# Kernel optimization log

Hardware: AMD Instinct MI355X
Metric: run time of the kernel (lower is better)

## Reference

```python
import jax, jax.numpy as jnp
import numpy as np

B, S, N, D, H = 128, 512, 32, 512, 2  # batch, seq_len, num_size, node_dim, hop_size
NPAD = 4  # padded number slots per row


def _lin(key, fi, fo):
    return 0.02 * jax.random.normal(key, (H, fi, fo), jnp.float32), jnp.zeros((H, fo), jnp.float32)


def setup_inputs() -> dict:
    key = jax.random.key(0)
    ks = jax.random.split(key, 12)
    encoder_outputs = jax.random.normal(ks[0], (S, B, D), jnp.float32)
    num_encoder_outputs = jax.random.normal(ks[1], (B, N, D), jnp.float32)
    # distinct positions per row in [0, S), last NPAD slots padded with -1
    num_pos_pad = jnp.argsort(jax.random.uniform(ks[2], (B, S)), axis=-1)[:, :N].astype(jnp.int32)
    num_pos_pad = num_pos_pad.at[:, -NPAD:].set(-1)
    # order ranks 1..N (random permutation per row), 0 on padded slots
    num_order_pad = (jnp.argsort(jax.random.uniform(ks[3], (B, N)), axis=-1) + 1).astype(jnp.int32)
    num_order_pad = num_order_pad.at[:, -NPAD:].set(0)
    w_n1a, b_n1a = _lin(ks[4], D, D)
    w_n1b, b_n1b = _lin(ks[5], D, D)
    w_n2a, b_n2a = _lin(ks[6], D, D)
    w_n2b, b_n2b = _lin(ks[7], D, D)
    w_g, b_g = _lin(ks[8], 4 * D, D)
    w_o, b_o = _lin(ks[9], 2 * D, D)
    return dict(encoder_outputs=encoder_outputs, num_encoder_outputs=num_encoder_outputs,
                num_pos_pad=num_pos_pad, num_order_pad=num_order_pad,
                w_n1a=w_n1a, b_n1a=b_n1a, w_n1b=w_n1b, b_n1b=b_n1b,
                w_n2a=w_n2a, b_n2a=b_n2a, w_n2b=w_n2b, b_n2b=b_n2b,
                w_g=w_g, b_g=b_g, w_o=w_o, b_o=b_o)


def reference(encoder_outputs, num_encoder_outputs, num_pos_pad, num_order_pad,
              w_n1a, b_n1a, w_n1b, b_n1b, w_n2a, b_n2a, w_n2b, b_n2b,
              w_g, b_g, w_o, b_o):
    node_mask = (num_order_pad > 0)                              # [B,N]
    greater = num_order_pad[:, :, None] > num_order_pad[:, None, :]
    lower = ~greater                                             # <=
    eye = jnp.eye(N, dtype=jnp.float32)
    pair = (node_mask[:, None, :] & node_mask[:, :, None]).astype(jnp.float32) * (1.0 - eye)
    g_gt = pair * greater.astype(jnp.float32) + eye              # [B,N,N]
    g_lt = pair * lower.astype(jnp.float32) + eye
    # row-normalize (D^{-1} A); diagonal guarantees row sums >= 1
    g_gt = g_gt / g_gt.sum(-1, keepdims=True)
    g_lt = g_lt / g_lt.sum(-1, keepdims=True)

    node = num_encoder_outputs                                   # [B,N,D]
    for h in range(H):
        ni1 = jax.nn.relu(jnp.einsum('bnm,bmd,de->bne', g_gt, node, w_n1a[h]) + b_n1a[h])
        ni1 = jax.nn.relu(jnp.einsum('bnm,bmd,de->bne', g_gt, ni1, w_n1b[h]) + b_n1b[h])
        ni2 = jax.nn.relu(jnp.einsum('bnm,bmd,de->bne', g_lt, node, w_n2a[h]) + b_n2a[h])
        ni2 = jax.nn.relu(jnp.einsum('bnm,bmd,de->bne', g_lt, ni2, w_n2b[h]) + b_n2b[h])
        gate_in = jnp.concatenate([ni1, ni2, ni1 + ni2, ni1 - ni2], axis=-1)
        gate = jax.nn.sigmoid(gate_in @ w_g[h] + b_g[h])
        node_info = gate * ni1 + (1.0 - gate) * ni2
        node = jax.nn.relu(jnp.concatenate([node, node_info], axis=-1) @ w_o[h] + b_o[h])

    # scatter node embeddings into padded [B, S+1, D]; pads -> slot S (dropped)
    num_mask = num_pos_pad > -1
    clamped = jnp.where(num_mask, num_pos_pad, S)                # [B,N]
    gnn_info = jnp.zeros((B, S + 1, D), jnp.float32)
    gnn_info = gnn_info.at[jnp.arange(B)[:, None], clamped].set(node)
    gnn_info = gnn_info[:, :S, :].transpose(1, 0, 2)             # [S,B,D]
    gnn_info = encoder_outputs + gnn_info
    num_embedding = num_encoder_outputs + node
    problem_output = jnp.max(gnn_info, axis=0)                   # [B,D]
    return gnn_info, num_embedding, problem_output
```

## Files before the change

kernel.cpp:

```cpp
#include <hip/hip_runtime.h>
#include <math.h>

#define BB 128
#define SS 512
#define NN 32
#define DD 512
#define HH 2
#define MM (BB * NN)
#define DSQ (DD * DD)

typedef short bf16x8 __attribute__((ext_vector_type(8)));
typedef float f32x4 __attribute__((ext_vector_type(4)));

__device__ __forceinline__ unsigned short f2bf(float f) {
    unsigned int u = __float_as_uint(f);
    u += 0x7fffu + ((u >> 16) & 1u);
    return (unsigned short)(u >> 16);
}
__device__ __forceinline__ float bf2f(unsigned short h) {
    return __uint_as_float(((unsigned int)h) << 16);
}
__device__ __forceinline__ void g2l16(const void* gp, void* lp) {
    __builtin_amdgcn_global_load_lds(
        (const __attribute__((address_space(1))) void*)gp,
        (__attribute__((address_space(3))) void*)lp, 16, 0, 0);
}

__global__ __launch_bounds__(256) void adj_k(const int* __restrict__ order,
                                             const int* __restrict__ pos,
                                             float* __restrict__ g_gt,
                                             float* __restrict__ g_lt,
                                             int* __restrict__ slot) {
    int b = blockIdx.x;
    __shared__ int ord[NN];
    __shared__ float sgt[NN][NN + 1];
    __shared__ float slt[NN][NN + 1];
    __shared__ float rs_gt[NN], rs_lt[NN];
    int tid = threadIdx.x;
    slot[b * SS + tid] = -1;
    slot[b * SS + 256 + tid] = -1;
    if (tid < NN) ord[tid] = order[b * NN + tid];
    __syncthreads();
    for (int q = 0; q < 4; ++q) {
        int idx = tid + 256 * q;
        int n = idx >> 5, m = idx & 31;
        bool valid = (ord[n] > 0) && (ord[m] > 0) && (n != m);
        float eye = (n == m) ? 1.f : 0.f;
        bool gt = ord[n] > ord[m];
        sgt[n][m] = ((valid && gt) ? 1.f : 0.f) + eye;
        slt[n][m] = ((valid && !gt) ? 1.f : 0.f) + eye;
    }
    __syncthreads();
    if (tid < NN) {
        float s1 = 0.f, s2 = 0.f;
        for (int m = 0; m < NN; ++m) { s1 += sgt[tid][m]; s2 += slt[tid][m]; }
        rs_gt[tid] = s1; rs_lt[tid] = s2;
    }
    __syncthreads();
    for (int q = 0; q < 4; ++q) {
        int idx = tid + 256 * q;
        int n = idx >> 5, m = idx & 31;
        g_gt[b * 1024 + idx] = sgt[n][m] / rs_gt[n];
        g_lt[b * 1024 + idx] = slt[n][m] / rs_lt[n];
    }
    if (tid < NN) {
        int p = pos[b * NN + tid];
        if (p >= 0) slot[b * SS + p] = tid;
    }
}

struct WSfull { const float* s[12]; int slot[12]; const float* w_g; };

__global__ __launch_bounds__(256) void wprep_k(WSfull w, unsigned short* __restrict__ Wt) {
    int which = blockIdx.x;
    int tile = blockIdx.y;
    int tr = (tile >> 3) * 64, tc = (tile & 7) * 64;
    __shared__ float c1[64][65];
    __shared__ float c2[64][65];
    int lc = threadIdx.x & 63, g4 = threadIdx.x >> 6;
    if (which < 12) {
        const float* src = w.s[which];
        unsigned short* dst = Wt + (size_t)w.slot[which] * DSQ;
        for (int i = 0; i < 16; ++i) {
            int lr = g4 * 16 + i;
            c1[lr][lc] = src[(size_t)(tr + lr) * DD + tc + lc];
        }
        __syncthreads();
        for (int i = 0; i < 16; ++i) {
            int lr = g4 * 16 + i;
            dst[(size_t)(tc + lr) * DD + tr + lc] = f2bf(c1[lc][lr]);
        }
    } else {
        int h = which - 12;
        const float* base = w.w_g + (size_t)h * 4 * DSQ;
        for (int i = 0; i < 16; ++i) {
            int lr = g4 * 16 + i;
            int k = tr + lr, n = tc + lc;
            float a  = base[(size_t)k * DD + n];
            float b2 = base[(size_t)(DD + k) * DD + n];
            float c  = base[(size_t)(2 * DD + k) * DD + n];
            float d4 = base[(size_t)(3 * DD + k) * DD + n];
            c1[lr][lc] = a + c + d4;
            c2[lr][lc] = b2 + c - d4;
        }
        __syncthreads();
        unsigned short* d1 = Wt + (size_t)(h * 8 + 4) * DSQ;
        unsigned short* d2 = Wt + (size_t)(h * 8 + 5) * DSQ;
        for (int i = 0; i < 16; ++i) {
            int lr = g4 * 16 + i;
            d1[(size_t)(tc + lr) * DD + tr + lc] = f2bf(c1[lc][lr]);
            d2[(size_t)(tc + lr) * DD + tr + lc] = f2bf(c2[lc][lr]);
        }
    }
}

__global__ void conv_k(const float* __restrict__ x, unsigned short* __restrict__ o) {
    size_t i = ((size_t)blockIdx.x * 256 + threadIdx.x) * 4;
    float4 v = *(const float4*)(x + i);
    ushort4 r;
    r.x = f2bf(v.x); r.y = f2bf(v.y); r.z = f2bf(v.z); r.w = f2bf(v.w);
    *(ushort4*)(o + i) = r;
}

struct GA {
    const unsigned short* A1; const unsigned short* W1;
    const unsigned short* A2; const unsigned short* W2;
    const float* g; const float* bias;
    const unsigned short* gin1; const unsigned short* gin2;
    unsigned short* out;
};

template <bool MIX, bool DUAL, bool GATE>
__global__ __launch_bounds__(256) void mgemm_k(GA a0, GA a1) {
    GA g = (blockIdx.z == 0) ? a0 : a1;
    __shared__ __align__(16) unsigned short stag[8192];
    __shared__ float gsh[2048];
    const int tid = threadIdx.x;
    const int lane = tid & 63;
    const int wave = tid >> 6;
    const int wr = wave & 1, wc = wave >> 1;
    const int bm = blockIdx.x * 64, bn = blockIdx.y * 64;

    if (MIX) {
        const float4* gsrc = (const float4*)(g.g + (size_t)(bm >> 5) * 1024);
        ((float4*)gsh)[tid] = gsrc[tid];
        ((float4*)gsh)[tid + 256] = gsrc[tid + 256];
    }

    f32x4 acc[2][2];
#pragma unroll
    for (int i = 0; i < 2; ++i)
#pragma unroll
        for (int j = 0; j < 2; ++j) {
            acc[i][j].x = 0.f; acc[i][j].y = 0.f; acc[i][j].z = 0.f; acc[i][j].w = 0.f;
        }

    const int r0 = tid >> 3,          s0 = (tid & 7) ^ (r0 & 7);
    const int r1 = (tid + 256) >> 3,  s1 = (tid & 7) ^ (r1 & 7);
    unsigned short* As = stag;
    unsigned short* Bs = stag + 4096;
    unsigned short* dA0 = As + wave * 512;
    unsigned short* dA1 = As + 2048 + wave * 512;
    unsigned short* dB0 = Bs + wave * 512;
    unsigned short* dB1 = Bs + 2048 + wave * 512;

    int aoff[2][2], boff[2][2];
#pragma unroll
    for (int t = 0; t < 2; ++t)
#pragma unroll
        for (int i = 0; i < 2; ++i) {
            int s = t * 4 + (lane >> 4);
            int p = s ^ (lane & 7);
            int m = wr * 32 + i * 16 + (lane & 15);
            aoff[t][i] = m * 64 + p * 8;
            int n = wc * 32 + i * 16 + (lane & 15);
            boff[t][i] = n * 64 + p * 8;
        }

    const int nsrc = DUAL ? 2 : 1;
    for (int src = 0; src < nsrc; ++src) {
        const unsigned short* A = src ? g.A2 : g.A1;
        const unsigned short* W = src ? g.W2 : g.W1;
        const unsigned short* Ab0 = A + (size_t)(bm + r0) * DD + s0 * 8;
        const unsigned short* Ab1 = A + (size_t)(bm + r1) * DD + s1 * 8;
        const unsigned short* Wb0 = W + (size_t)(bn + r0) * DD + s0 * 8;
        const unsigned short* Wb1 = W + (size_t)(bn + r1) * DD + s1 * 8;
        for (int k0 = 0; k0 < DD; k0 += 64) {
            g2l16(Ab0 + k0, dA0);
            g2l16(Ab1 + k0, dA1);
            g2l16(Wb0 + k0, dB0);
            g2l16(Wb1 + k0, dB1);
            __syncthreads();
            bf16x8 af[2][2], bf_[2][2];
#pragma unroll
            for (int t = 0; t < 2; ++t)
#pragma unroll
                for (int i = 0; i < 2; ++i) {
                    af[t][i]  = *(const bf16x8*)(As + aoff[t][i]);
                    bf_[t][i] = *(const bf16x8*)(Bs + boff[t][i]);
                }
#pragma unroll
            for (int t = 0; t < 2; ++t)
#pragma unroll
                for (int i = 0; i < 2; ++i)
#pragma unroll
                    for (int j = 0; j < 2; ++j)
                        acc[i][j] = __builtin_amdgcn_mfma_f32_16x16x32_bf16(
                            af[t][i], bf_[t][j], acc[i][j], 0, 0, 0);
            __syncthreads();
        }
    }

    if (!MIX) {
#pragma unroll
        for (int i = 0; i < 2; ++i) {
            int row = bm + wr * 32 + i * 16 + (lane >> 4) * 4;
#pragma unroll
            for (int j = 0; j < 2; ++j) {
                int col = bn + wc * 32 + j * 16 + (lane & 15);
                float bv = g.bias[col];
#pragma unroll
                for (int rg = 0; rg < 4; ++rg) {
                    float v = acc[i][j][rg] + bv;
                    size_t idx = (size_t)(row + rg) * DD + col;
                    if (GATE) {
                        float gg = 1.f / (1.f + __expf(-v));
                        float x1 = bf2f(g.gin1[idx]);
                        float x2 = bf2f(g.gin2[idx]);
                        g.out[idx] = f2bf(gg * x1 + (1.f - gg) * x2);
                    } else {
                        g.out[idx] = f2bf(fmaxf(v, 0.f));
                    }
                }
            }
        }
    } else {
        float* S = (float*)stag;
#pragma unroll
        for (int i = 0; i < 2; ++i) {
            int row = wr * 32 + i * 16 + (lane >> 4) * 4;
#pragma unroll
            for (int j = 0; j < 2; ++j) {
                int col = wc * 32 + j * 16 + (lane & 15);
#pragma unroll
                for (int rg = 0; rg < 4; ++rg) S[(row + rg) * 64 + col] = acc[i][j][rg];
            }
        }
        __syncthreads();
#pragma unroll
        for (int t = 0; t < 4; ++t) {
            int task = t * 256 + tid;
            int n = task >> 4, dq = task & 15;
            int bt = n >> 5, nl = n & 31;
            float r0m = 0.f, r1m = 0.f, r2m = 0.f, r3m = 0.f;
            const float* gr = gsh + bt * 1024 + nl * 32;
            const float* Sb = S + bt * 32 * 64 + dq * 4;
#pragma unroll
            for (int m = 0; m < 32; ++m) {
                float gv = gr[m];
                f32x4 sv = *(const f32x4*)(Sb + m * 64);
                r0m += gv * sv.x; r1m += gv * sv.y; r2m += gv * sv.z; r3m += gv * sv.w;
            }
            float4 bv = *(const float4*)(g.bias + bn + dq * 4);
            ushort4 ov;
            ov.x = f2bf(fmaxf(r0m + bv.x, 0.f));
            ov.y = f2bf(fmaxf(r1m + bv.y, 0.f));
            ov.z = f2bf(fmaxf(r2m + bv.z, 0.f));
            ov.w = f2bf(fmaxf(r3m + bv.w, 0.f));
            *(ushort4*)(g.out + (size_t)(bm + n) * DD + bn + dq * 4) = ov;
        }
    }
}

__global__ __launch_bounds__(256) void gnn_k(const float* __restrict__ enc,
                                             const unsigned short* __restrict__ node,
                                             const int* __restrict__ slot,
                                             const float* __restrict__ num_enc,
                                             float* __restrict__ out_gnn,
                                             float* __restrict__ out_nemb,
                                             float* __restrict__ partial) {
    int b = blockIdx.x;
    int t = threadIdx.x;
    if (blockIdx.y >= 16) {
        int q = blockIdx.y - 16;
        size_t base = (size_t)b * NN * DD + (size_t)q * (NN * DD / 4);
        for (int it = 0; it < 4; ++it) {
            size_t i = base + (size_t)(it * 256 + t) * 4;
            float4 a = *(const float4*)(num_enc + i);
            ushort4 nb = *(const ushort4*)(node + i);
            float4 r;
            r.x = a.x + bf2f(nb.x);
            r.y = a.y + bf2f(nb.y);
            r.z = a.z + bf2f(nb.z);
            r.w = a.w + bf2f(nb.w);
            *(float4*)(out_nemb + i) = r;
        }
        return;
    }
    __shared__ int sl[32];
    __shared__ float4 red[128];
    int s0 = blockIdx.y * 32;
    if (t < 32) sl[t] = slot[b * SS + s0 + t];
    __syncthreads();
    const int dv = (t & 127) * 4;
    const int sh = t >> 7;
    float4 mx = {-INFINITY, -INFINITY, -INFINITY, -INFINITY};
#pragma unroll 4
    for (int i = 0; i < 16; ++i) {
        int sloc = sh * 16 + i;
        int s = s0 + sloc;
        int n = sl[sloc];
        size_t ebase = ((size_t)s * BB + b) * DD + dv;
        float4 v = *(const float4*)(enc + ebase);
        if (n >= 0) {
            ushort4 nb = *(const ushort4*)(node + ((size_t)b * NN + n) * DD + dv);
            v.x += bf2f(nb.x);
            v.y += bf2f(nb.y);
            v.z += bf2f(nb.z);
            v.w += bf2f(nb.w);
        }
        *(float4*)(out_gnn + ebase) = v;
        mx.x = fmaxf(mx.x, v.x);
        mx.y = fmaxf(mx.y, v.y);
        mx.z = fmaxf(mx.z, v.z);
        mx.w = fmaxf(mx.w, v.w);
    }
    if (sh == 1) red[t & 127] = mx;
    __syncthreads();
    if (sh == 0) {
        float4 o = red[t];
        mx.x = fmaxf(mx.x, o.x);
        mx.y = fmaxf(mx.y, o.y);
        mx.z = fmaxf(mx.z, o.z);
        mx.w = fmaxf(mx.w, o.w);
        *(float4*)(partial + ((size_t)b * 16 + blockIdx.y) * DD + dv) = mx;
    }
}

__global__ void pmax_k(const float* __restrict__ partial, float* __restrict__ out_prob) {
    int i = blockIdx.x * 256 + threadIdx.x;
    if (i >= BB * DD) return;
    int b = i >> 9, d = i & 511;
    float m = -INFINITY;
    for (int c = 0; c < 16; ++c) m = fmaxf(m, partial[((size_t)b * 16 + c) * DD + d]);
    out_prob[i] = m;
}

extern "C" void kernel_launch(void* const* d_in, const int* in_sizes, int n_in,
                              void* d_out, int out_size, void* d_ws, size_t ws_size,
                              hipStream_t stream) {
    const float* enc     = (const float*)d_in[0];
    const float* num_enc = (const float*)d_in[1];
    const int*   pos     = (const int*)d_in[2];
    const int*   order   = (const int*)d_in[3];
    const float* w_n1a = (const float*)d_in[4];  const float* b_n1a = (const float*)d_in[5];
    const float* w_n1b = (const float*)d_in[6];  const float* b_n1b = (const float*)d_in[7];
    const float* w_n2a = (const float*)d_in[8];  const float* b_n2a = (const float*)d_in[9];
    const float* w_n2b = (const float*)d_in[10]; const float* b_n2b = (const float*)d_in[11];
    const float* w_g   = (const float*)d_in[12]; const float* b_g   = (const float*)d_in[13];
    const float* w_o   = (const float*)d_in[14]; const float* b_o   = (const float*)d_in[15];

    char* wp = (char*)d_ws;
    float* g_gt = (float*)wp;        wp += (size_t)BB * NN * NN * 4;
    float* g_lt = (float*)wp;        wp += (size_t)BB * NN * NN * 4;
    float* partial = (float*)wp;     wp += (size_t)BB * 16 * DD * 4;
    int* slot = (int*)wp;            wp += (size_t)BB * SS * 4;
    unsigned short* Wt = (unsigned short*)wp;    wp += (size_t)16 * DSQ * 2;
    unsigned short* node0 = (unsigned short*)wp; wp += (size_t)MM * DD * 2;
    unsigned short* nodeA = (unsigned short*)wp; wp += (size_t)MM * DD * 2;
    unsigned short* nodeB = (unsigned short*)wp; wp += (size_t)MM * DD * 2;
    unsigned short* ni1 = (unsigned short*)wp;   wp += (size_t)MM * DD * 2;
    unsigned short* ni2 = (unsigned short*)wp;   wp += (size_t)MM * DD * 2;
    unsigned short* t1 = (unsigned short*)wp;    wp += (size_t)MM * DD * 2;
    unsigned short* t2 = (unsigned short*)wp;    wp += (size_t)MM * DD * 2;

    float* out_gnn  = (float*)d_out;
    float* out_nemb = out_gnn + (size_t)SS * BB * DD;
    float* out_prob = out_nemb + (size_t)BB * NN * DD;

    adj_k<<<BB, 256, 0, stream>>>(order, pos, g_gt, g_lt, slot);

    WSfull wsrc;
    const float* srcs[12] = {w_n1a, w_n1b, w_n2a, w_n2b, w_o, w_o + DSQ,
                             w_n1a + DSQ, w_n1b + DSQ, w_n2a + DSQ, w_n2b + DSQ,
                             w_o + 2 * DSQ, w_o + 3 * DSQ};
    int slots[12] = {0, 1, 2, 3, 6, 7, 8, 9, 10, 11, 14, 15};
    for (int i = 0; i < 12; ++i) { wsrc.s[i] = srcs[i]; wsrc.slot[i] = slots[i]; }
    wsrc.w_g = w_g;
    wprep_k<<<dim3(14, 64), 256, 0, stream>>>(wsrc, Wt);
    conv_k<<<(MM * DD) / 1024, 256, 0, stream>>>(num_enc, node0);

    dim3 dgrid(MM / 64, DD / 64, 2);
    dim3 sgrid(MM / 64, DD / 64, 1);

    const unsigned short* nodeIn = node0;
    for (int h = 0; h < HH; ++h) {
        unsigned short* nodeOut = (h == 0) ? nodeA : nodeB;
        const unsigned short* Wh = Wt + (size_t)h * 8 * DSQ;

        GA sa0 = {nodeIn, Wh + 0 * DSQ, nullptr, nullptr, g_gt, b_n1a + h * DD,
                  nullptr, nullptr, ni1};
        GA sa1 = {nodeIn, Wh + 2 * DSQ, nullptr, nullptr, g_lt, b_n2a + h * DD,
                  nullptr, nullptr, ni2};
        mgemm_k<true, false, false><<<dgrid, 256, 0, stream>>>(sa0, sa1);

        GA sb0 = {ni1, Wh + 1 * DSQ, nullptr, nullptr, g_gt, b_n1b + h * DD,
                  nullptr, nullptr, t1};
        GA sb1 = {ni2, Wh + 3 * DSQ, nullptr, nullptr, g_lt, b_n2b + h * DD,
                  nullptr, nullptr, t2};
        mgemm_k<true, false, false><<<dgrid, 256, 0, stream>>>(sb0, sb1);

        GA gg = {t1, Wh + 4 * DSQ, t2, Wh + 5 * DSQ, nullptr, b_g + h * DD, t1, t2, ni1};
        mgemm_k<false, true, true><<<sgrid, 256, 0, stream>>>(gg, gg);

        GA go = {nodeIn, Wh + 6 * DSQ, ni1, Wh + 7 * DSQ, nullptr, b_o + h * DD,
                 nullptr, nullptr, nodeOut};
        mgemm_k<false, true, false><<<sgrid, 256, 0, stream>>>(go, go);

        nodeIn = nodeOut;
    }
    const unsigned short* nodeF = nodeIn;

    gnn_k<<<dim3(BB, 20), 256, 0, stream>>>(enc, nodeF, slot, num_enc,
                                            out_gnn, out_nemb, partial);
    pmax_k<<<(BB * DD) / 256, 256, 0, stream>>>(partial, out_prob);
}
```

Before: 412.1 us.

## Split adjacency mixing into separate kernel and enlarge GEMM tiles to 128x128

Moves the per-batch adjacency mixing (G @ X) out of the GEMM epilogue into a standalone mix_k kernel that runs before each GEMM. The mixing order changes from (X W) then G to (G X) then W. This lets the GEMM tiles grow from 64x64 to 128x128 with a 4x4 MFMA accumulator per wave, which raises data reuse per loaded tile. In exchange it adds two extra kernel launches per hop plus an extra bf16 round trip for the mixed activations. The larger tiles also use more registers and LDS and leave only 256 or 128 blocks per GEMM.

```diff
diff --git a/kernel.cpp b/kernel.cpp
--- a/kernel.cpp
+++ b/kernel.cpp
@@ -122,58 +122,111 @@
     *(ushort4*)(o + i) = r;
 }
 
+__global__ __launch_bounds__(256) void mix_k(const float* __restrict__ g_gt,
+                                             const float* __restrict__ g_lt,
+                                             const unsigned short* __restrict__ X1,
+                                             const unsigned short* __restrict__ X2,
+                                             unsigned short* __restrict__ Z1,
+                                             unsigned short* __restrict__ Z2) {
+    const int b = blockIdx.x;
+    const int dc = blockIdx.y * 128;
+    const float* G = blockIdx.z ? g_lt : g_gt;
+    const unsigned short* X = blockIdx.z ? X2 : X1;
+    unsigned short* Z = blockIdx.z ? Z2 : Z1;
+    __shared__ float gs[NN * 33];
+    __shared__ float xs[NN][128];
+    const int t = threadIdx.x;
+    {
+        float4 v = ((const float4*)(G + (size_t)b * 1024))[t];
+        int n = t >> 3, m0 = (t & 7) * 4;
+        float* gp = gs + n * 33 + m0;
+        gp[0] = v.x; gp[1] = v.y; gp[2] = v.z; gp[3] = v.w;
+    }
+#pragma unroll
+    for (int q = 0; q < 2; ++q) {
+        int e = t + 256 * q;
+        int m = e >> 4, c = (e & 15) * 8;
+        const unsigned short* src = X + ((size_t)(b * NN + m)) * DD + dc + c;
+        ushort4 lo = *(const ushort4*)src;
+        ushort4 hi = *(const ushort4*)(src + 4);
+        float* xp = &xs[m][c];
+        xp[0] = bf2f(lo.x); xp[1] = bf2f(lo.y); xp[2] = bf2f(lo.z); xp[3] = bf2f(lo.w);
+        xp[4] = bf2f(hi.x); xp[5] = bf2f(hi.y); xp[6] = bf2f(hi.z); xp[7] = bf2f(hi.w);
+    }
+    __syncthreads();
+    const int n = t >> 3;
+    const int c0 = (t & 7) * 16;
+    f32x4 r0 = {0.f, 0.f, 0.f, 0.f}, r1 = r0, r2 = r0, r3 = r0;
+#pragma unroll
+    for (int m = 0; m < NN; ++m) {
+        float gv = gs[n * 33 + m];
+        const float* xr = &xs[m][c0];
+        r0 += gv * *(const f32x4*)(xr);
+        r1 += gv * *(const f32x4*)(xr + 4);
+        r2 += gv * *(const f32x4*)(xr + 8);
+        r3 += gv * *(const f32x4*)(xr + 12);
+    }
+    unsigned short* dst = Z + ((size_t)(b * NN + n)) * DD + dc + c0;
+    ushort4 o0, o1, o2, o3;
+    o0.x = f2bf(r0.x); o0.y = f2bf(r0.y); o0.z = f2bf(r0.z); o0.w = f2bf(r0.w);
+    o1.x = f2bf(r1.x); o1.y = f2bf(r1.y); o1.z = f2bf(r1.z); o1.w = f2bf(r1.w);
+    o2.x = f2bf(r2.x); o2.y = f2bf(r2.y); o2.z = f2bf(r2.z); o2.w = f2bf(r2.w);
+    o3.x = f2bf(r3.x); o3.y = f2bf(r3.y); o3.z = f2bf(r3.z); o3.w = f2bf(r3.w);
+    *(ushort4*)(dst)      = o0;
+    *(ushort4*)(dst + 4)  = o1;
+    *(ushort4*)(dst + 8)  = o2;
+    *(ushort4*)(dst + 12) = o3;
+}
+
 struct GA {
     const unsigned short* A1; const unsigned short* W1;
     const unsigned short* A2; const unsigned short* W2;
-    const float* g; const float* bias;
+    const float* bias;
     const unsigned short* gin1; const unsigned short* gin2;
     unsigned short* out;
 };
 
-template <bool MIX, bool DUAL, bool GATE>
+template <bool DUAL, bool GATE>
 __global__ __launch_bounds__(256) void mgemm_k(GA a0, GA a1) {
     GA g = (blockIdx.z == 0) ? a0 : a1;
-    __shared__ __align__(16) unsigned short stag[8192];
-    __shared__ float gsh[2048];
+    __shared__ __align__(16) unsigned short As[128 * 64];
+    __shared__ __align__(16) unsigned short Bs[128 * 64];
     const int tid = threadIdx.x;
     const int lane = tid & 63;
     const int wave = tid >> 6;
     const int wr = wave & 1, wc = wave >> 1;
-    const int bm = blockIdx.x * 64, bn = blockIdx.y * 64;
-
-    if (MIX) {
-        const float4* gsrc = (const float4*)(g.g + (size_t)(bm >> 5) * 1024);
-        ((float4*)gsh)[tid] = gsrc[tid];
-        ((float4*)gsh)[tid + 256] = gsrc[tid + 256];
-    }
-
-    f32x4 acc[2][2];
-#pragma unroll
-    for (int i = 0; i < 2; ++i)
-#pragma unroll
-        for (int j = 0; j < 2; ++j) {
+    const int bm = blockIdx.x * 128, bn = blockIdx.y * 128;
+
+    f32x4 acc[4][4];
+#pragma unroll
+    for (int i = 0; i < 4; ++i)
+#pragma unroll
+        for (int j = 0; j < 4; ++j) {
             acc[i][j].x = 0.f; acc[i][j].y = 0.f; acc[i][j].z = 0.f; acc[i][j].w = 0.f;
         }
 
-    const int r0 = tid >> 3,          s0 = (tid & 7) ^ (r0 & 7);
-    const int r1 = (tid + 256) >> 3,  s1 = (tid & 7) ^ (r1 & 7);
-    unsigned short* As = stag;
-    unsigned short* Bs = stag + 4096;
-    unsigned short* dA0 = As + wave * 512;
-    unsigned short* dA1 = As + 2048 + wave * 512;
-    unsigned short* dB0 = Bs + wave * 512;
-    unsigned short* dB1 = Bs + 2048 + wave * 512;
-
-    int aoff[2][2], boff[2][2];
+    int rr[4], ss[4];
+    unsigned short* dA[4];
+    unsigned short* dB[4];
+#pragma unroll
+    for (int q = 0; q < 4; ++q) {
+        int e = tid + 256 * q;
+        rr[q] = e >> 3;
+        ss[q] = (tid & 7) ^ (rr[q] & 7);
+        dA[q] = As + (size_t)e * 8;
+        dB[q] = Bs + (size_t)e * 8;
+    }
+
+    int aoff[2][4], boff[2][4];
 #pragma unroll
     for (int t = 0; t < 2; ++t)
 #pragma unroll
-        for (int i = 0; i < 2; ++i) {
-            int s = t * 4 + (lane >> 4);
-            int p = s ^ (lane & 7);
-            int m = wr * 32 + i * 16 + (lane & 15);
+        for (int i = 0; i < 4; ++i) {
+            int sl = t * 4 + (lane >> 4);
+            int p = sl ^ (lane & 7);
+            int m = wr * 64 + i * 16 + (lane & 15);
             aoff[t][i] = m * 64 + p * 8;
-            int n = wc * 32 + i * 16 + (lane & 15);
+            int n = wc * 64 + i * 16 + (lane & 15);
             boff[t][i] = n * 64 + p * 8;
         }
 
@@ -181,93 +234,59 @@
     for (int src = 0; src < nsrc; ++src) {
         const unsigned short* A = src ? g.A2 : g.A1;
         const unsigned short* W = src ? g.W2 : g.W1;
-        const unsigned short* Ab0 = A + (size_t)(bm + r0) * DD + s0 * 8;
-        const unsigned short* Ab1 = A + (size_t)(bm + r1) * DD + s1 * 8;
-        const unsigned short* Wb0 = W + (size_t)(bn + r0) * DD + s0 * 8;
-        const unsigned short* Wb1 = W + (size_t)(bn + r1) * DD + s1 * 8;
+        const unsigned short* pa[4];
+        const unsigned short* pb[4];
+#pragma unroll
+        for (int q = 0; q < 4; ++q) {
+            pa[q] = A + (size_t)(bm + rr[q]) * DD + ss[q] * 8;
+            pb[q] = W + (size_t)(bn + rr[q]) * DD + ss[q] * 8;
+        }
         for (int k0 = 0; k0 < DD; k0 += 64) {
-            g2l16(Ab0 + k0, dA0);
-            g2l16(Ab1 + k0, dA1);
-            g2l16(Wb0 + k0, dB0);
-            g2l16(Wb1 + k0, dB1);
+#pragma unroll
+            for (int q = 0; q < 4; ++q) g2l16(pa[q] + k0, dA[q]);
+#pragma unroll
+            for (int q = 0; q < 4; ++q) g2l16(pb[q] + k0, dB[q]);
             __syncthreads();
-            bf16x8 af[2][2], bf_[2][2];
+            bf16x8 af[2][4], bf_[2][4];
 #pragma unroll
             for (int t = 0; t < 2; ++t)
 #pragma unroll
-                for (int i = 0; i < 2; ++i) {
+                for (int i = 0; i < 4; ++i) {
                     af[t][i]  = *(const bf16x8*)(As + aoff[t][i]);
                     bf_[t][i] = *(const bf16x8*)(Bs + boff[t][i]);
                 }
 #pragma unroll
             for (int t = 0; t < 2; ++t)
 #pragma unroll
-                for (int i = 0; i < 2; ++i)
-#pragma unroll
-                    for (int j = 0; j < 2; ++j)
+                for (int i = 0; i < 4; ++i)
+#pragma unroll
+                    for (int j = 0; j < 4; ++j)
                         acc[i][j] = __builtin_amdgcn_mfma_f32_16x16x32_bf16(
                             af[t][i], bf_[t][j], acc[i][j], 0, 0, 0);
             __syncthreads();
         }
     }
 
-    if (!MIX) {
-#pragma unroll
-        for (int i = 0; i < 2; ++i) {
-            int row = bm + wr * 32 + i * 16 + (lane >> 4) * 4;
-#pragma unroll
-            for (int j = 0; j < 2; ++j) {
-                int col = bn + wc * 32 + j * 16 + (lane & 15);
-                float bv = g.bias[col];
-#pragma unroll
-                for (int rg = 0; rg < 4; ++rg) {
-                    float v = acc[i][j][rg] + bv;
-                    size_t idx = (size_t)(row + rg) * DD + col;
-                    if (GATE) {
-                        float gg = 1.f / (1.f + __expf(-v));
-                        float x1 = bf2f(g.gin1[idx]);
-                        float x2 = bf2f(g.gin2[idx]);
-                        g.out[idx] = f2bf(gg * x1 + (1.f - gg) * x2);
-                    } else {
-                        g.out[idx] = f2bf(fmaxf(v, 0.f));
-                    }
+#pragma unroll
+    for (int i = 0; i < 4; ++i) {
+        int row = bm + wr * 64 + i * 16 + (lane >> 4) * 4;
+#pragma unroll
+        for (int j = 0; j < 4; ++j) {
+            int col = bn + wc * 64 + j * 16 + (lane & 15);
+            float bv = g.bias[col];
+#pragma unroll
+            for (int rg = 0; rg < 4; ++rg) {
+                float v = acc[i][j][rg] + bv;
+                size_t idx = (size_t)(row + rg) * DD + col;
+                if (GATE) {
+                    float gg = 1.f / (1.f + __expf(-v));
+                    float x1 = bf2f(g.gin1[idx]);
+                    float x2 = bf2f(g.gin2[idx]);
+                    g.out[idx] = f2bf(gg * x1 + (1.f - gg) * x2);
+                } else {
+                    g.out[idx] = f2bf(fmaxf(v, 0.f));
                 }
             }
-        }
-    } else {
-        float* S = (float*)stag;
-#pragma unroll
-        for (int i = 0; i < 2; ++i) {
-            int row = wr * 32 + i * 16 + (lane >> 4) * 4;
-#pragma unroll
-            for (int j = 0; j < 2; ++j) {
-                int col = wc * 32 + j * 16 + (lane & 15);
-#pragma unroll
-                for (int rg = 0; rg < 4; ++rg) S[(row + rg) * 64 + col] = acc[i][j][rg];
-            }
-        }
-        __syncthreads();
-#pragma unroll
-        for (int t = 0; t < 4; ++t) {
-            int task = t * 256 + tid;
-            int n = task >> 4, dq = task & 15;
-            int bt = n >> 5, nl = n & 31;
-            float r0m = 0.f, r1m = 0.f, r2m = 0.f, r3m = 0.f;
-            const float* gr = gsh + bt * 1024 + nl * 32;
-            const float* Sb = S + bt * 32 * 64 + dq * 4;
-#pragma unroll
-            for (int m = 0; m < 32; ++m) {
-                float gv = gr[m];
-                f32x4 sv = *(const f32x4*)(Sb + m * 64);
-                r0m += gv * sv.x; r1m += gv * sv.y; r2m += gv * sv.z; r3m += gv * sv.w;
-            }
-            float4 bv = *(const float4*)(g.bias + bn + dq * 4);
-            ushort4 ov;
-            ov.x = f2bf(fmaxf(r0m + bv.x, 0.f));
-            ov.y = f2bf(fmaxf(r1m + bv.y, 0.f));
-            ov.z = f2bf(fmaxf(r2m + bv.z, 0.f));
-            ov.w = f2bf(fmaxf(r3m + bv.w, 0.f));
-            *(ushort4*)(g.out + (size_t)(bm + n) * DD + bn + dq * 4) = ov;
         }
     }
 }
@@ -390,32 +409,33 @@
     wprep_k<<<dim3(14, 64), 256, 0, stream>>>(wsrc, Wt);
     conv_k<<<(MM * DD) / 1024, 256, 0, stream>>>(num_enc, node0);
 
-    dim3 dgrid(MM / 64, DD / 64, 2);
-    dim3 sgrid(MM / 64, DD / 64, 1);
+    dim3 ggrid(32, 4, 2);
+    dim3 sgrid(32, 4, 1);
+    dim3 mgrid(BB, 4, 2);
 
     const unsigned short* nodeIn = node0;
     for (int h = 0; h < HH; ++h) {
         unsigned short* nodeOut = (h == 0) ? nodeA : nodeB;
+        unsigned short* zb1 = (h == 0) ? nodeB : node0;
+        unsigned short* zb2 = (unsigned short*)partial;
         const unsigned short* Wh = Wt + (size_t)h * 8 * DSQ;
 
-        GA sa0 = {nodeIn, Wh + 0 * DSQ, nullptr, nullptr, g_gt, b_n1a + h * DD,
-                  nullptr, nullptr, ni1};
-        GA sa1 = {nodeIn, Wh + 2 * DSQ, nullptr, nullptr, g_lt, b_n2a + h * DD,
-                  nullptr, nullptr, ni2};
-        mgemm_k<true, false, false><<<dgrid, 256, 0, stream>>>(sa0, sa1);
-
-        GA sb0 = {ni1, Wh + 1 * DSQ, nullptr, nullptr, g_gt, b_n1b + h * DD,
-                  nullptr, nullptr, t1};
-        GA sb1 = {ni2, Wh + 3 * DSQ, nullptr, nullptr, g_lt, b_n2b + h * DD,
-                  nullptr, nullptr, t2};
-        mgemm_k<true, false, false><<<dgrid, 256, 0, stream>>>(sb0, sb1);
-
-        GA gg = {t1, Wh + 4 * DSQ, t2, Wh + 5 * DSQ, nullptr, b_g + h * DD, t1, t2, ni1};
-        mgemm_k<false, true, true><<<sgrid, 256, 0, stream>>>(gg, gg);
-
-        GA go = {nodeIn, Wh + 6 * DSQ, ni1, Wh + 7 * DSQ, nullptr, b_o + h * DD,
+        mix_k<<<mgrid, 256, 0, stream>>>(g_gt, g_lt, nodeIn, nodeIn, t1, t2);
+        GA sa0 = {t1, Wh + 0 * DSQ, nullptr, nullptr, b_n1a + h * DD, nullptr, nullptr, ni1};
+        GA sa1 = {t2, Wh + 2 * DSQ, nullptr, nullptr, b_n2a + h * DD, nullptr, nullptr, ni2};
+        mgemm_k<false, false><<<ggrid, 256, 0, stream>>>(sa0, sa1);
+
+        mix_k<<<mgrid, 256, 0, stream>>>(g_gt, g_lt, ni1, ni2, zb1, zb2);
+        GA sb0 = {zb1, Wh + 1 * DSQ, nullptr, nullptr, b_n1b + h * DD, nullptr, nullptr, t1};
+        GA sb1 = {zb2, Wh + 3 * DSQ, nullptr, nullptr, b_n2b + h * DD, nullptr, nullptr, t2};
+        mgemm_k<false, false><<<ggrid, 256, 0, stream>>>(sb0, sb1);
+
+        GA gg = {t1, Wh + 4 * DSQ, t2, Wh + 5 * DSQ, b_g + h * DD, t1, t2, ni1};
+        mgemm_k<true, true><<<sgrid, 256, 0, stream>>>(gg, gg);
+
+        GA go = {nodeIn, Wh + 6 * DSQ, ni1, Wh + 7 * DSQ, b_o + h * DD,
                  nullptr, nullptr, nodeOut};
-        mgemm_k<false, true, false><<<sgrid, 256, 0, stream>>>(go, go);
+        mgemm_k<true, false><<<sgrid, 256, 0, stream>>>(go, go);
 
         nodeIn = nodeOut;
     }
```

New measurement: 474.5 us. +15.1%, slower.
